# Kernel tuning notes

Measured on AMD Instinct MI355X. Metric: run time of the kernel, lower is better.

Reference implementation:

```python
import jax, jax.numpy as jnp
import numpy as np

EMBED_DIM = 1024
NUM_HEADS = 16
HEAD_DIM = EMBED_DIM // NUM_HEADS


def setup_inputs() -> dict:
    key = jax.random.key(0)
    k1, k2, k3, k4, k5 = jax.random.split(key, 5)
    B, N, D = 2, 2048, EMBED_DIM
    s = 1.0 / np.sqrt(D)
    x = jax.random.normal(k1, (B, N, D), dtype=jnp.float32)
    qkv_w = jax.random.uniform(k2, (3 * D, D), minval=-s, maxval=s, dtype=jnp.float32)
    qkv_b = jax.random.uniform(k3, (3 * D,), minval=-s, maxval=s, dtype=jnp.float32)
    proj_w = jax.random.uniform(k4, (D, D), minval=-s, maxval=s, dtype=jnp.float32)
    proj_b = jax.random.uniform(k5, (D,), minval=-s, maxval=s, dtype=jnp.float32)
    return {"x": x, "qkv_w": qkv_w, "qkv_b": qkv_b, "proj_w": proj_w, "proj_b": proj_b}


def reference(x, qkv_w, qkv_b, proj_w, proj_b):
    B, N, D = x.shape
    H, Hd = NUM_HEADS, HEAD_DIM
    scale = Hd ** (-0.5)
    # QKV projection (torch Linear: x @ W.T + b)
    qkv = x @ qkv_w.T + qkv_b                      # [B, N, 3D]
    q, k, v = jnp.split(qkv, 3, axis=-1)
    def split_heads(t):
        return t.reshape(B, N, H, Hd).transpose(0, 2, 1, 3)  # [B, H, N, Hd]
    q, k, v = map(split_heads, (q, k, v))
    attn = jnp.einsum("bhqd,bhkd->bhqk", q, k) * scale       # [B, H, N, N]
    attn = jax.nn.softmax(attn, axis=-1)
    out = jnp.einsum("bhqk,bhkd->bhqd", attn, v)             # [B, H, N, Hd]
    out = out.transpose(0, 2, 1, 3).reshape(B, N, D)
    return out @ proj_w.T + proj_b
```

## Files before the change

### kernel.cpp

```cpp
#include <hip/hip_runtime.h>
#include <hip/hip_bf16.h>


#define DEV __device__ __forceinline__

typedef __attribute__((ext_vector_type(8))) __bf16 bf16x8;
typedef __attribute__((ext_vector_type(4))) float f32x4;

static DEV unsigned short f2bf(float f) {
  unsigned u = __builtin_bit_cast(unsigned, f);
  u += 0x7FFFu + ((u >> 16) & 1u);
  return (unsigned short)(u >> 16);
}

static DEV float fexp2(float x) {
#if __has_builtin(__builtin_amdgcn_exp2f)
  return __builtin_amdgcn_exp2f(x);
#else
  return __expf(x * 0.69314718055994531f);
#endif
}

static DEV float max3(float a, float b, float c) {
  return fmaxf(fmaxf(a, b), c);
}

static DEV void gld16(const void* g, void* l) {
  __builtin_amdgcn_global_load_lds(
      (const __attribute__((address_space(1))) unsigned int*)g,
      (__attribute__((address_space(3))) unsigned int*)l, 16, 0, 0);
}

static DEV f32x4 mfma16(bf16x8 a, bf16x8 b, f32x4 c) {
  return __builtin_amdgcn_mfma_f32_16x16x32_bf16(a, b, c, 0, 0, 0);
}

__global__ void k_conv(const float* __restrict__ x, const float* __restrict__ qw,
                       const float* __restrict__ pw, unsigned short* __restrict__ xb,
                       unsigned short* __restrict__ wqb, unsigned short* __restrict__ pwb) {
  int b = blockIdx.x;
  const float* s;
  unsigned short* d;
  int base;
  if (b < 4096)      { s = x;  d = xb;  base = b; }
  else if (b < 7168) { s = qw; d = wqb; base = b - 4096; }
  else               { s = pw; d = pwb; base = b - 7168; }
  int i = (base * 256 + threadIdx.x) * 4;
  float4 v = *reinterpret_cast<const float4*>(s + i);
  union { unsigned short h[4]; uint2 u; } cv;
  cv.h[0] = f2bf(v.x); cv.h[1] = f2bf(v.y); cv.h[2] = f2bf(v.z); cv.h[3] = f2bf(v.w);
  *reinterpret_cast<uint2*>(d + i) = cv.u;
}

static DEV void gemm_tile(const unsigned short* __restrict__ Asb,
                          const unsigned short* __restrict__ Bsb,
                          int wm, int wn, int fr, int fg, f32x4 (&acc)[4][4]) {
  bf16x8 af[4], bw[4];
#pragma unroll
  for (int m = 0; m < 4; ++m)
    af[m] = *reinterpret_cast<const bf16x8*>(Asb + (wm * 64 + m * 16 + fr) * 32 + fg * 8);
#pragma unroll
  for (int n = 0; n < 4; ++n)
    bw[n] = *reinterpret_cast<const bf16x8*>(Bsb + (wn * 64 + n * 16 + fr) * 32 + fg * 8);
#pragma unroll
  for (int m = 0; m < 4; ++m)
#pragma unroll
    for (int n = 0; n < 4; ++n)
      acc[m][n] = mfma16(af[m], bw[n], acc[m][n]);
}

#define QSTAGE(ab, k0)                                                        \
  {                                                                           \
    _Pragma("unroll")                                                         \
    for (int c = 0; c < 2; ++c) {                                             \
      int bi = c * 4096 + wid * 1024 + lane * 16;                             \
      int row = bi >> 6, ce = (bi & 63) >> 1;                                 \
      gld16(gA + (size_t)row * K + (k0) + ce, &As[ab][c * 2048 + wid * 512]); \
      gld16(gW + (size_t)row * K + (k0) + ce, &Bs[ab][c * 2048 + wid * 512]); \
    }                                                                         \
  }

__global__ __launch_bounds__(256) void k_qkv(
    const unsigned short* __restrict__ A, const unsigned short* __restrict__ W,
    const float* __restrict__ bias, unsigned short* __restrict__ Qb,
    unsigned short* __restrict__ Kb, unsigned short* __restrict__ Vt) {
  const int K = 1024;
  __shared__ __align__(16) unsigned short As[2][128 * 32], Bs[2][128 * 32];
  const int tid = threadIdx.x, lane = tid & 63, wid = tid >> 6;
  const int wm = wid >> 1, wn = wid & 1, fr = lane & 15, fg = lane >> 4;
  const size_t bm = blockIdx.x, bn = blockIdx.y;
  const unsigned short* gA = A + bm * 128 * K;
  const unsigned short* gW = W + bn * 128 * K;
  f32x4 acc[4][4] = {};
  QSTAGE(0, 0);
  __syncthreads();
  for (int i = 0; i < 16; ++i) {
    QSTAGE(1, i * 64 + 32);
    gemm_tile(As[0], Bs[0], wm, wn, fr, fg, acc);
    __syncthreads();
    if (i < 15) QSTAGE(0, i * 64 + 64);
    gemm_tile(As[1], Bs[1], wm, wn, fr, fg, acc);
    __syncthreads();
  }
  const float QSCALE = 0.18033688011112043f;
  float bv[4];
#pragma unroll
  for (int n = 0; n < 4; ++n) bv[n] = bias[bn * 128 + wn * 64 + n * 16 + fr];
#pragma unroll
  for (int m = 0; m < 4; ++m)
#pragma unroll
    for (int n = 0; n < 4; ++n) {
      int f = (int)bn * 128 + wn * 64 + n * 16 + fr;
      int t = f >> 10, d = f & 1023, h = d >> 6, hd = d & 63;
      int token0 = (int)bm * 128 + wm * 64 + m * 16 + fg * 4;
      int b_ = token0 >> 11, nn0 = token0 & 2047;
      size_t bh = (size_t)(b_ * 16 + h);
      float v0 = acc[m][n][0] + bv[n], v1 = acc[m][n][1] + bv[n];
      float v2 = acc[m][n][2] + bv[n], v3 = acc[m][n][3] + bv[n];
      if (t == 0) {
        unsigned short* q = Qb + (bh * 2048 + nn0) * 64 + hd;
        q[0] = f2bf(v0 * QSCALE); q[64] = f2bf(v1 * QSCALE);
        q[128] = f2bf(v2 * QSCALE); q[192] = f2bf(v3 * QSCALE);
      } else if (t == 1) {
        unsigned short* k = Kb + (bh * 2048 + nn0) * 64 + hd;
        k[0] = f2bf(v0); k[64] = f2bf(v1); k[128] = f2bf(v2); k[192] = f2bf(v3);
      } else {
        union { unsigned short h[4]; uint2 u; } pk;
        pk.h[0] = f2bf(v0); pk.h[1] = f2bf(v1);
        pk.h[2] = f2bf(v2); pk.h[3] = f2bf(v3);
        *reinterpret_cast<uint2*>(Vt + (bh * 64 + hd) * 2048 + nn0) = pk.u;
      }
    }
}

static DEV void attn_tile(const unsigned short* __restrict__ Ksb,
                          const unsigned short* __restrict__ Vsb,
                          unsigned short* __restrict__ pw, const bf16x8* qf,
                          int fr, int fg, const int* kcol, const int* pcol,
                          f32x4* accO, float& mrow, float& lpart) {
  const int prow = fr * 64;
  f32x4 s[4] = {};
  __builtin_amdgcn_s_setprio(1);
#pragma unroll
  for (int nf = 0; nf < 4; ++nf)
#pragma unroll
    for (int ks = 0; ks < 2; ++ks) {
      bf16x8 kf = *reinterpret_cast<const bf16x8*>(&Ksb[(nf * 16 + fr) * 64 + kcol[ks]]);
      s[nf] = mfma16(kf, qf[ks], s[nf]);
    }
  __builtin_amdgcn_s_setprio(0);
  bf16x8 vf[2][4];
#pragma unroll
  for (int ks = 0; ks < 2; ++ks)
#pragma unroll
    for (int df = 0; df < 4; ++df)
      vf[ks][df] = *reinterpret_cast<const bf16x8*>(&Vsb[(df * 16 + fr) * 64 + kcol[ks]]);
  float m0 = max3(s[0][0], s[0][1], s[0][2]);
  float m1 = max3(s[0][3], s[1][0], s[1][1]);
  float m2 = max3(s[1][2], s[1][3], s[2][0]);
  float m3 = max3(s[2][1], s[2][2], s[2][3]);
  float m4 = max3(s[3][0], s[3][1], s[3][2]);
  float mymax = fmaxf(max3(m0, m1, m2), max3(m3, m4, s[3][3]));
  if (!__all(mymax <= mrow + 8.0f)) {
    float pmax = fmaxf(mymax, __shfl_xor(mymax, 16));
    pmax = fmaxf(pmax, __shfl_xor(pmax, 32));
    float mnew = fmaxf(mrow, pmax);
    float sc = fexp2(mrow - mnew);
    mrow = mnew;
    lpart *= sc;
    float scq[4];
#pragma unroll
    for (int r = 0; r < 4; ++r) scq[r] = __shfl(sc, fg * 4 + r);
#pragma unroll
    for (int df = 0; df < 4; ++df)
#pragma unroll
      for (int r = 0; r < 4; ++r) accO[df][r] *= scq[r];
  }
  float rsn[4];
#pragma unroll
  for (int nf = 0; nf < 4; ++nf) {
    float p0 = fexp2(s[nf][0] - mrow), p1 = fexp2(s[nf][1] - mrow);
    float p2 = fexp2(s[nf][2] - mrow), p3 = fexp2(s[nf][3] - mrow);
    union { unsigned short h[4]; uint2 u; } pk;
    pk.h[0] = f2bf(p0); pk.h[1] = f2bf(p1); pk.h[2] = f2bf(p2); pk.h[3] = f2bf(p3);
    rsn[nf] = (p0 + p1) + (p2 + p3);
    *reinterpret_cast<uint2*>(&pw[prow + pcol[nf]]) = pk.u;
  }
  lpart += (rsn[0] + rsn[1]) + (rsn[2] + rsn[3]);
  bf16x8 pf[2];
#pragma unroll
  for (int ks = 0; ks < 2; ++ks)
    pf[ks] = *reinterpret_cast<const bf16x8*>(&pw[prow + kcol[ks]]);
  __builtin_amdgcn_s_setprio(1);
#pragma unroll
  for (int df = 0; df < 4; ++df)
#pragma unroll
    for (int ks = 0; ks < 2; ++ks)
      accO[df] = mfma16(pf[ks], vf[ks][df], accO[df]);
  __builtin_amdgcn_s_setprio(0);
}

__global__ __launch_bounds__(256) void k_attn(
    const unsigned short* __restrict__ Qb, const unsigned short* __restrict__ Kb,
    const unsigned short* __restrict__ Vt, unsigned short* __restrict__ Ob) {
  __shared__ __align__(16) unsigned short Ks0[64 * 64], Ks1[64 * 64];
  __shared__ __align__(16) unsigned short Vs0[64 * 64], Vs1[64 * 64];
  __shared__ __align__(16) unsigned short p_lds[4][16 * 64];
  const int tid = threadIdx.x, lane = tid & 63, w = tid >> 6;
  const int fr = lane & 15, fg = lane >> 4;
  const int bid = (int)(blockIdx.x & 7) * 128 + (int)(blockIdx.x >> 3);
  const int qt = bid & 31, bh = bid >> 5;
  const unsigned short* Qp = Qb + ((size_t)bh * 2048 + qt * 64 + w * 16) * 64;
  const unsigned short* Kp = Kb + (size_t)bh * 2048 * 64;
  const unsigned short* Vp = Vt + (size_t)bh * 64 * 2048;
  unsigned short* pw = &p_lds[w][0];

  int kcol[2], pcol[4];
#pragma unroll
  for (int ks = 0; ks < 2; ++ks) kcol[ks] = ((ks * 4 + fg) ^ (fr & 7)) * 8;
#pragma unroll
  for (int nf = 0; nf < 4; ++nf)
    pcol[nf] = (((2 * nf + (fg >> 1)) ^ (fr & 7)) * 8) + (fg & 1) * 4;

  const int crow0 = w * 16 + (lane >> 3);
  bf16x8 qf[2];
#pragma unroll
  for (int ks = 0; ks < 2; ++ks)
    qf[ks] = *reinterpret_cast<const bf16x8*>(Qp + fr * 64 + ks * 32 + fg * 8);

  f32x4 accO[4] = {};
  float mrow = -1e30f, lpart = 0.f;

#define STAGE(KDST, VDST, kti)                                                \
  {                                                                           \
    const unsigned short* Kt_ = Kp + (kti) * 64 * 64;                         \
    _Pragma("unroll")                                                         \
    for (int j = 0; j < 2; ++j) {                                             \
      int cr = crow0 + j * 8;                                                 \
      int cs = (lane & 7) ^ (cr & 7);                                         \
      gld16(Kt_ + cr * 64 + cs * 8, (KDST) + (w * 2 + j) * 512);              \
      gld16(Vp + (size_t)cr * 2048 + (kti) * 64 + cs * 8,                     \
            (VDST) + (w * 2 + j) * 512);                                      \
    }                                                                         \
  }

  STAGE(Ks0, Vs0, 0);
  STAGE(Ks1, Vs1, 1);
  __syncthreads();
  for (int i = 0; i < 16; ++i) {
    attn_tile(Ks0, Vs0, pw, qf, fr, fg, kcol, pcol, accO, mrow, lpart);
    __syncthreads();
    if (i < 15) STAGE(Ks0, Vs0, 2 * i + 2);
    attn_tile(Ks1, Vs1, pw, qf, fr, fg, kcol, pcol, accO, mrow, lpart);
    __syncthreads();
    if (i < 15) STAGE(Ks1, Vs1, 2 * i + 3);
  }
#undef STAGE
  float lrow = lpart;
  lrow += __shfl_xor(lrow, 16);
  lrow += __shfl_xor(lrow, 32);
  float linv = 1.f / lrow;
  float lq[4];
#pragma unroll
  for (int r = 0; r < 4; ++r) lq[r] = __shfl(linv, fg * 4 + r);
  const int b_ = bh >> 4, h = bh & 15;
#pragma unroll
  for (int df = 0; df < 4; ++df)
#pragma unroll
    for (int r = 0; r < 4; ++r) {
      int nn = qt * 64 + w * 16 + fg * 4 + r;
      int d = df * 16 + fr;
      Ob[(size_t)(b_ * 2048 + nn) * 1024 + h * 64 + d] = f2bf(accO[df][r] * lq[r]);
    }
}

__global__ __launch_bounds__(256) void k_proj(
    const unsigned short* __restrict__ A, const unsigned short* __restrict__ W,
    const float* __restrict__ bias, float* __restrict__ out) {
  const int K = 1024;
  __shared__ __align__(16) unsigned short As[2][128 * 32], Bs[2][128 * 32];
  const int tid = threadIdx.x, lane = tid & 63, wid = tid >> 6;
  const int wm = wid >> 1, wn = wid & 1, fr = lane & 15, fg = lane >> 4;
  const size_t bm = blockIdx.x, bn = blockIdx.y;
  const unsigned short* gA = A + bm * 128 * K;
  const unsigned short* gW = W + bn * 128 * K;
  f32x4 acc[4][4] = {};
  QSTAGE(0, 0);
  __syncthreads();
  for (int i = 0; i < 16; ++i) {
    QSTAGE(1, i * 64 + 32);
    gemm_tile(As[0], Bs[0], wm, wn, fr, fg, acc);
    __syncthreads();
    if (i < 15) QSTAGE(0, i * 64 + 64);
    gemm_tile(As[1], Bs[1], wm, wn, fr, fg, acc);
    __syncthreads();
  }
  float bv[4];
#pragma unroll
  for (int n = 0; n < 4; ++n) bv[n] = bias[bn * 128 + wn * 64 + n * 16 + fr];
#pragma unroll
  for (int m = 0; m < 4; ++m)
#pragma unroll
    for (int n = 0; n < 4; ++n)
#pragma unroll
      for (int r = 0; r < 4; ++r) {
        size_t token = bm * 128 + wm * 64 + m * 16 + fg * 4 + r;
        int f = (int)bn * 128 + wn * 64 + n * 16 + fr;
        out[token * 1024 + f] = acc[m][n][r] + bv[n];
      }
}

extern "C" void kernel_launch(void* const* d_in, const int* in_sizes, int n_in,
                              void* d_out, int out_size, void* d_ws, size_t ws_size,
                              hipStream_t stream) {
  const float* x      = (const float*)d_in[0];
  const float* qkv_w  = (const float*)d_in[1];
  const float* qkv_b  = (const float*)d_in[2];
  const float* proj_w = (const float*)d_in[3];
  const float* proj_b = (const float*)d_in[4];
  float* out = (float*)d_out;
  char* ws = (char*)d_ws;
  unsigned short* xb  = (unsigned short*)(ws);
  unsigned short* wqb = (unsigned short*)(ws + (size_t)(8u << 20));
  unsigned short* pwb = (unsigned short*)(ws + (size_t)(14u << 20));
  unsigned short* Qb  = (unsigned short*)(ws + (size_t)(16u << 20));
  unsigned short* Kb  = (unsigned short*)(ws + (size_t)(24u << 20));
  unsigned short* Vt  = (unsigned short*)(ws + (size_t)(32u << 20));
  unsigned short* Ob  = (unsigned short*)(ws + (size_t)(40u << 20));

  k_conv<<<8192, 256, 0, stream>>>(x, qkv_w, proj_w, xb, wqb, pwb);
  k_qkv<<<dim3(32, 24), 256, 0, stream>>>(xb, wqb, qkv_b, Qb, Kb, Vt);
  k_attn<<<1024, 256, 0, stream>>>(Qb, Kb, Vt, Ob);
  k_proj<<<dim3(32, 8), 256, 0, stream>>>(Ob, pwb, proj_b, out);
}
```

Before: 217.2 us.

## Drop LDS double buffering in GEMMs and load V directly from global

The QKV and projection GEMMs go from a two-stage LDS ping-pong to a single buffer, with a load, barrier, compute, barrier sequence on each k-step. The attention kernel stops staging V tiles in shared memory and reads V fragments straight from global memory inside the tile routine. This cuts LDS use and staging instructions, but removes the overlap of loads with MFMA work and makes V reads uncached global accesses on the critical path. It looks like a simplification or regression experiment rather than a targeted speedup.

Result: slower. 293.4 us (+35.0%).

```diff
diff --git a/kernel.cpp b/kernel.cpp
--- a/kernel.cpp
+++ b/kernel.cpp
@@ -69,14 +69,14 @@
       acc[m][n] = mfma16(af[m], bw[n], acc[m][n]);
 }
 
-#define QSTAGE(ab, k0)                                                        \
+#define QSTAGE(k0)                                                            \
   {                                                                           \
     _Pragma("unroll")                                                         \
     for (int c = 0; c < 2; ++c) {                                             \
       int bi = c * 4096 + wid * 1024 + lane * 16;                             \
       int row = bi >> 6, ce = (bi & 63) >> 1;                                 \
-      gld16(gA + (size_t)row * K + (k0) + ce, &As[ab][c * 2048 + wid * 512]); \
-      gld16(gW + (size_t)row * K + (k0) + ce, &Bs[ab][c * 2048 + wid * 512]); \
+      gld16(gA + (size_t)row * K + (k0) + ce, As + c * 2048 + wid * 512);     \
+      gld16(gW + (size_t)row * K + (k0) + ce, Bs + c * 2048 + wid * 512);     \
     }                                                                         \
   }
 
@@ -85,21 +85,17 @@
     const float* __restrict__ bias, unsigned short* __restrict__ Qb,
     unsigned short* __restrict__ Kb, unsigned short* __restrict__ Vt) {
   const int K = 1024;
-  __shared__ __align__(16) unsigned short As[2][128 * 32], Bs[2][128 * 32];
+  __shared__ __align__(16) unsigned short As[128 * 32], Bs[128 * 32];
   const int tid = threadIdx.x, lane = tid & 63, wid = tid >> 6;
   const int wm = wid >> 1, wn = wid & 1, fr = lane & 15, fg = lane >> 4;
   const size_t bm = blockIdx.x, bn = blockIdx.y;
   const unsigned short* gA = A + bm * 128 * K;
   const unsigned short* gW = W + bn * 128 * K;
   f32x4 acc[4][4] = {};
-  QSTAGE(0, 0);
-  __syncthreads();
-  for (int i = 0; i < 16; ++i) {
-    QSTAGE(1, i * 64 + 32);
-    gemm_tile(As[0], Bs[0], wm, wn, fr, fg, acc);
-    __syncthreads();
-    if (i < 15) QSTAGE(0, i * 64 + 64);
-    gemm_tile(As[1], Bs[1], wm, wn, fr, fg, acc);
+  for (int k0 = 0; k0 < K; k0 += 32) {
+    QSTAGE(k0);
+    __syncthreads();
+    gemm_tile(As, Bs, wm, wn, fr, fg, acc);
     __syncthreads();
   }
   const float QSCALE = 0.18033688011112043f;
@@ -134,7 +130,7 @@
 }
 
 static DEV void attn_tile(const unsigned short* __restrict__ Ksb,
-                          const unsigned short* __restrict__ Vsb,
+                          const unsigned short* __restrict__ Vp, int kt,
                           unsigned short* __restrict__ pw, const bf16x8* qf,
                           int fr, int fg, const int* kcol, const int* pcol,
                           f32x4* accO, float& mrow, float& lpart) {
@@ -154,7 +150,8 @@
   for (int ks = 0; ks < 2; ++ks)
 #pragma unroll
     for (int df = 0; df < 4; ++df)
-      vf[ks][df] = *reinterpret_cast<const bf16x8*>(&Vsb[(df * 16 + fr) * 64 + kcol[ks]]);
+      vf[ks][df] = *reinterpret_cast<const bf16x8*>(
+          Vp + (size_t)(df * 16 + fr) * 2048 + kt * 64 + ks * 32 + fg * 8);
   float m0 = max3(s[0][0], s[0][1], s[0][2]);
   float m1 = max3(s[0][3], s[1][0], s[1][1]);
   float m2 = max3(s[1][2], s[1][3], s[2][0]);
@@ -204,7 +201,6 @@
     const unsigned short* __restrict__ Qb, const unsigned short* __restrict__ Kb,
     const unsigned short* __restrict__ Vt, unsigned short* __restrict__ Ob) {
   __shared__ __align__(16) unsigned short Ks0[64 * 64], Ks1[64 * 64];
-  __shared__ __align__(16) unsigned short Vs0[64 * 64], Vs1[64 * 64];
   __shared__ __align__(16) unsigned short p_lds[4][16 * 64];
   const int tid = threadIdx.x, lane = tid & 63, w = tid >> 6;
   const int fr = lane & 15, fg = lane >> 4;
@@ -231,7 +227,7 @@
   f32x4 accO[4] = {};
   float mrow = -1e30f, lpart = 0.f;
 
-#define STAGE(KDST, VDST, kti)                                                \
+#define STAGE(KDST, kti)                                                      \
   {                                                                           \
     const unsigned short* Kt_ = Kp + (kti) * 64 * 64;                         \
     _Pragma("unroll")                                                         \
@@ -239,21 +235,19 @@
       int cr = crow0 + j * 8;                                                 \
       int cs = (lane & 7) ^ (cr & 7);                                         \
       gld16(Kt_ + cr * 64 + cs * 8, (KDST) + (w * 2 + j) * 512);              \
-      gld16(Vp + (size_t)cr * 2048 + (kti) * 64 + cs * 8,                     \
-            (VDST) + (w * 2 + j) * 512);                                      \
     }                                                                         \
   }
 
-  STAGE(Ks0, Vs0, 0);
-  STAGE(Ks1, Vs1, 1);
+  STAGE(Ks0, 0);
+  STAGE(Ks1, 1);
   __syncthreads();
   for (int i = 0; i < 16; ++i) {
-    attn_tile(Ks0, Vs0, pw, qf, fr, fg, kcol, pcol, accO, mrow, lpart);
-    __syncthreads();
-    if (i < 15) STAGE(Ks0, Vs0, 2 * i + 2);
-    attn_tile(Ks1, Vs1, pw, qf, fr, fg, kcol, pcol, accO, mrow, lpart);
-    __syncthreads();
-    if (i < 15) STAGE(Ks1, Vs1, 2 * i + 3);
+    attn_tile(Ks0, Vp, 2 * i, pw, qf, fr, fg, kcol, pcol, accO, mrow, lpart);
+    __syncthreads();
+    if (i < 15) STAGE(Ks0, 2 * i + 2);
+    attn_tile(Ks1, Vp, 2 * i + 1, pw, qf, fr, fg, kcol, pcol, accO, mrow, lpart);
+    __syncthreads();
+    if (i < 15) STAGE(Ks1, 2 * i + 3);
   }
 #undef STAGE
   float lrow = lpart;
@@ -278,21 +272,17 @@
     const unsigned short* __restrict__ A, const unsigned short* __restrict__ W,
     const float* __restrict__ bias, float* __restrict__ out) {
   const int K = 1024;
-  __shared__ __align__(16) unsigned short As[2][128 * 32], Bs[2][128 * 32];
+  __shared__ __align__(16) unsigned short As[128 * 32], Bs[128 * 32];
   const int tid = threadIdx.x, lane = tid & 63, wid = tid >> 6;
   const int wm = wid >> 1, wn = wid & 1, fr = lane & 15, fg = lane >> 4;
   const size_t bm = blockIdx.x, bn = blockIdx.y;
   const unsigned short* gA = A + bm * 128 * K;
   const unsigned short* gW = W + bn * 128 * K;
   f32x4 acc[4][4] = {};
-  QSTAGE(0, 0);
-  __syncthreads();
-  for (int i = 0; i < 16; ++i) {
-    QSTAGE(1, i * 64 + 32);
-    gemm_tile(As[0], Bs[0], wm, wn, fr, fg, acc);
-    __syncthreads();
-    if (i < 15) QSTAGE(0, i * 64 + 64);
-    gemm_tile(As[1], Bs[1], wm, wn, fr, fg, acc);
+  for (int k0 = 0; k0 < K; k0 += 32) {
+    QSTAGE(k0);
+    __syncthreads();
+    gemm_tile(As, Bs, wm, wn, fr, fg, acc);
     __syncthreads();
   }
   float bv[4];
```
